# Kernel optimization log

Hardware: AMD Instinct MI355X
Metric: run time of the kernel (lower is better)

The kernel has to match this reference:

```python
import jax, jax.numpy as jnp
import numpy as np

D_MODEL = 1024
NUM_HEADS_Q = 16
NUM_HEADS_KV = 1
D_HEAD = D_MODEL // NUM_HEADS_Q  # 64
KV_DIM = D_HEAD * NUM_HEADS_KV   # 64


def setup_inputs() -> dict:
    key = jax.random.key(0)
    ks = jax.random.split(key, 9)
    b, n = 4, 2048
    s_in = 1.0 / np.sqrt(D_MODEL)
    s_o = 1.0 / np.sqrt(D_MODEL)
    return {
        "x": jax.random.normal(ks[0], (b, n, D_MODEL), jnp.float32),
        # weights stored as [in, out] (= torch Linear weight transposed)
        "W_q": jax.random.uniform(ks[1], (D_MODEL, D_MODEL), jnp.float32, -s_in, s_in),
        "b_q": jax.random.uniform(ks[2], (D_MODEL,), jnp.float32, -s_in, s_in),
        "W_k": jax.random.uniform(ks[3], (D_MODEL, KV_DIM), jnp.float32, -s_in, s_in),
        "b_k": jax.random.uniform(ks[4], (KV_DIM,), jnp.float32, -s_in, s_in),
        "W_v": jax.random.uniform(ks[5], (D_MODEL, KV_DIM), jnp.float32, -s_in, s_in),
        "b_v": jax.random.uniform(ks[6], (KV_DIM,), jnp.float32, -s_in, s_in),
        "W_o": jax.random.uniform(ks[7], (D_MODEL, D_MODEL), jnp.float32, -s_o, s_o),
        "b_o": jax.random.uniform(ks[8], (D_MODEL,), jnp.float32, -s_o, s_o),
    }


def reference(x, W_q, b_q, W_k, b_k, W_v, b_v, W_o, b_o):
    b, n, d_model = x.shape
    # projections
    q = (x @ W_q + b_q).reshape(b, n, NUM_HEADS_Q, D_HEAD).transpose(0, 2, 1, 3)  # [b,hq,n,dh]
    k = (x @ W_k + b_k).reshape(b, n, NUM_HEADS_KV, D_HEAD).transpose(0, 2, 1, 3)  # [b,hkv,n,dh]
    v = (x @ W_v + b_v).reshape(b, n, NUM_HEADS_KV, D_HEAD).transpose(0, 2, 1, 3)
    # MQA: single KV head broadcast over query heads via einsum broadcasting
    scale = 1.0 / np.sqrt(D_HEAD).astype(np.float32)
    # scores [b,hq,n,n]; k/v have hkv=1, broadcast over hq
    scores = jnp.einsum("bhqd,bknd->bhqn", q, k)[..., 0, :, :][:, :, None] if False else None
    # cleaner: squeeze kv head (num_heads_kv == 1)
    k1 = k[:, 0]  # [b,n,dh]
    v1 = v[:, 0]  # [b,n,dh]
    scores = jnp.einsum("bhqd,bkd->bhqk", q, k1) * scale  # [b,hq,n,n]
    attn = jax.nn.softmax(scores, axis=-1)
    out = jnp.einsum("bhqk,bkd->bhqd", attn, v1)  # [b,hq,n,dh]
    out = out.transpose(0, 2, 1, 3).reshape(b, n, d_model)
    return out @ W_o + b_o
```

## Files before the change

### kernel.cpp

```cpp
#include <hip/hip_runtime.h>

using bf16x8 = __attribute__((ext_vector_type(8))) short;
using f32x4  = __attribute__((ext_vector_type(4))) float;
using u32x2  = __attribute__((ext_vector_type(2))) unsigned int;

__device__ __forceinline__ unsigned short f2bf(float f) {
  unsigned int u = __float_as_uint(f);
  u = u + 0x7fffu + ((u >> 16) & 1u);
  return (unsigned short)(u >> 16);
}

#if __has_builtin(__builtin_amdgcn_exp2f)
#define EXP2(x) __builtin_amdgcn_exp2f(x)
#else
#define EXP2(x) __expf((x) * 0.69314718056f)
#endif

__device__ __forceinline__ unsigned int cvt_pk_bf16(float lo, float hi) {
  unsigned int r;
  asm("v_cvt_pk_bf16_f32 %0, %1, %2" : "=v"(r) : "v"(lo), "v"(hi));
  return r;
}

#define GLL16(SRC, DST) __builtin_amdgcn_global_load_lds( \
    (const __attribute__((address_space(1))) unsigned int*)(SRC), \
    (__attribute__((address_space(3))) unsigned int*)(DST), 16, 0, 0)

__global__ void cvt_x_kernel(const float* __restrict__ x, unsigned short* __restrict__ xb, int n4) {
  int i = blockIdx.x * blockDim.x + threadIdx.x;
  if (i >= n4) return;
  const float4 v = reinterpret_cast<const float4*>(x)[i];
  ushort2 o0 = { f2bf(v.x), f2bf(v.y) };
  ushort2 o1 = { f2bf(v.z), f2bf(v.w) };
  reinterpret_cast<ushort2*>(xb)[2 * i]     = o0;
  reinterpret_cast<ushort2*>(xb)[2 * i + 1] = o1;
}

__global__ __launch_bounds__(256) void cvt_wt_kernel(
    const float* __restrict__ W, unsigned short* __restrict__ Wt, int N, int K) {
  __shared__ float tile[32][33];
  const int n0 = blockIdx.x * 32, k0 = blockIdx.y * 32;
  const int tx = threadIdx.x & 31, ty = threadIdx.x >> 5;
  #pragma unroll
  for (int i = 0; i < 32; i += 8)
    tile[ty + i][tx] = W[(size_t)(k0 + ty + i) * N + n0 + tx];
  __syncthreads();
  #pragma unroll
  for (int i = 0; i < 32; i += 8)
    Wt[(size_t)(n0 + ty + i) * K + k0 + tx] = f2bf(tile[tx][ty + i]);
}

template<int MODE>
__global__ __launch_bounds__(256) void gemm_kernel(
    const unsigned short* __restrict__ A, const unsigned short* __restrict__ Bt,
    const float* __restrict__ bias0, const float* __restrict__ bias1,
    const float* __restrict__ bias2,
    void* __restrict__ out0, void* __restrict__ out1, void* __restrict__ out2,
    int K, int N) {
  __shared__ __align__(16) unsigned short alds[2][128 * 32];
  __shared__ __align__(16) unsigned short blds[2][128 * 32];

  const int t    = threadIdx.x;
  const int lane = t & 63;
  const int wid  = t >> 6;
  const int lr = lane & 15, lg = lane >> 4;
  const int row0 = blockIdx.x * 128;
  const int col0 = blockIdx.y * 128;

  const size_t ldb = (size_t)K * 2;
  const char* Ag = (const char*)A  + (size_t)(row0 + (t >> 2)) * ldb + ((t & 3) << 4);
  const char* Bg = (const char*)Bt + (size_t)(col0 + (t >> 2)) * ldb + ((t & 3) << 4);
  char* adst = (char*)alds[0] + wid * 1024;
  char* bdst = (char*)blds[0] + wid * 1024;

  auto stage = [&](int buf, int k0) {
    const size_t kb = (size_t)k0 * 2;
    #pragma unroll
    for (int c = 0; c < 2; ++c) {
      GLL16(Ag + (size_t)c * 64 * ldb + kb, adst + buf * 8192 + c * 4096);
      GLL16(Bg + (size_t)c * 64 * ldb + kb, bdst + buf * 8192 + c * 4096);
    }
  };

  f32x4 acc[4][4];
  #pragma unroll
  for (int i = 0; i < 4; ++i)
    #pragma unroll
    for (int j = 0; j < 4; ++j)
      #pragma unroll
      for (int r = 0; r < 4; ++r) acc[i][j][r] = 0.f;

  stage(0, 0);
  __syncthreads();

  for (int step = 0; step < 32; ++step) {
    const int cur = step & 1;
    if (step < 31) stage(cur ^ 1, (step + 1) * 32);

    const char* ab = (const char*)alds[cur] + (wid >> 1) * 4096;
    const char* bb = (const char*)blds[cur] + (wid & 1) * 4096;
    bf16x8 am[4], bn[4];
    #pragma unroll
    for (int i = 0; i < 4; ++i)
      am[i] = *reinterpret_cast<const bf16x8*>(ab + (i * 16 + lr) * 64 + lg * 16);
    #pragma unroll
    for (int j = 0; j < 4; ++j)
      bn[j] = *reinterpret_cast<const bf16x8*>(bb + (j * 16 + lr) * 64 + lg * 16);
    #pragma unroll
    for (int i = 0; i < 4; ++i)
      #pragma unroll
      for (int j = 0; j < 4; ++j)
        acc[i][j] = __builtin_amdgcn_mfma_f32_16x16x32_bf16(am[i], bn[j], acc[i][j], 0, 0, 0);

    __syncthreads();
  }

  const int wrow0 = row0 + (wid >> 1) * 64;
  const int wcol0 = col0 + (wid & 1) * 64;
  #pragma unroll
  for (int i = 0; i < 4; ++i) {
    #pragma unroll
    for (int j = 0; j < 4; ++j) {
      const int col = wcol0 + j * 16 + lr;
      float bias;
      if constexpr (MODE == 0)
        bias = (col < 1024) ? bias0[col] : ((col < 1088) ? bias1[col - 1024] : bias2[col - 1088]);
      else
        bias = bias0[col];
      #pragma unroll
      for (int r = 0; r < 4; ++r) {
        const int row = wrow0 + i * 16 + lg * 4 + r;
        float v = acc[i][j][r] + bias;
        if constexpr (MODE == 0) {
          const int b = row >> 11, n = row & 2047;
          if (col < 1024) {
            v *= 0.180336880111f;
            const int h = col >> 6, d = col & 63;
            ((unsigned short*)out0)[(((b * 16 + h) * 2048) + n) * 64 + d] = f2bf(v);
          } else if (col < 1088) {
            ((unsigned short*)out1)[row * 64 + (col - 1024)] = f2bf(v);
          } else {
            ((unsigned short*)out2)[(b * 64 + (col - 1088)) * 2048 + n] = f2bf(v);
          }
        } else {
          ((float*)out0)[(size_t)row * N + col] = v;
        }
      }
    }
  }
}

__global__ __launch_bounds__(512, 4) void attn_kernel(
    const unsigned short* __restrict__ Q,
    const unsigned short* __restrict__ Kb,
    const unsigned short* __restrict__ Vt,
    unsigned short* __restrict__ Ao) {
  __shared__ __align__(16) unsigned short klds[2][64 * 64];
  __shared__ __align__(16) unsigned short vlds[2][64 * 64];
  __shared__ __align__(16) unsigned short plds[8][32 * 64];

  const int lane = threadIdx.x & 63;
  const int wid  = threadIdx.x >> 6;
  const int lr = lane & 15, lg = lane >> 4;
  const int lr7x16 = (lr & 7) << 4;
  const int bh = blockIdx.y, b = bh >> 4, h = bh & 15;
  const int q0 = blockIdx.x * 256 + wid * 32;

  const unsigned short* Qb = Q + (size_t)bh * 2048 * 64;
  const char* Kbase = (const char*)(Kb + (size_t)b * 2048 * 64);
  const char* Vbase = (const char*)(Vt + (size_t)b * 64 * 2048);

  const int srow  = lane >> 3;
  const int schnk = (lane & 7) ^ (srow & 7);
  const int krow  = wid * 8 + srow;
  const int koff_lane = krow * 128  + schnk * 16;
  const int voff_lane = krow * 4096 + schnk * 16;
  char* kdst = (char*)klds[0] + wid * 1024;
  char* vdst = (char*)vlds[0] + wid * 1024;

  auto stage = [&](int buf, int kt) {
    GLL16(Kbase + (size_t)kt * 8192 + koff_lane, kdst + buf * 8192);
    GLL16(Vbase + (size_t)kt * 128  + voff_lane, vdst + buf * 8192);
  };

  bf16x8 qa[2][2];
  #pragma unroll
  for (int iq = 0; iq < 2; ++iq)
    #pragma unroll
    for (int kc = 0; kc < 2; ++kc)
      qa[iq][kc] = *reinterpret_cast<const bf16x8*>(
          &Qb[(q0 + iq * 16 + lr) * 64 + kc * 32 + lg * 8]);

  float lsum[2] = {0.f, 0.f};
  f32x4 o[2][4];
  #pragma unroll
  for (int iq = 0; iq < 2; ++iq)
    #pragma unroll
    for (int dt = 0; dt < 4; ++dt)
      #pragma unroll
      for (int r = 0; r < 4; ++r) o[iq][dt][r] = 0.f;

  stage(0, 0);
  __syncthreads();

  for (int kt = 0; kt < 32; ++kt) {
    const int cur = kt & 1;
    if (kt < 31) stage(cur ^ 1, kt + 1);

    const char* kb8 = (const char*)klds[cur];
    const char* vb8 = (const char*)vlds[cur];
    char* pw = (char*)plds[wid];

    f32x4 s[2][4];
    #pragma unroll
    for (int iq = 0; iq < 2; ++iq)
      #pragma unroll
      for (int ct = 0; ct < 4; ++ct)
        #pragma unroll
        for (int r = 0; r < 4; ++r) s[iq][ct][r] = 0.f;

    #pragma unroll
    for (int kc = 0; kc < 2; ++kc) {
      bf16x8 kf[4];
      #pragma unroll
      for (int ct = 0; ct < 4; ++ct)
        kf[ct] = *reinterpret_cast<const bf16x8*>(
            kb8 + ((ct * 16 + lr) << 7) + ((((kc << 2) + lg) << 4) ^ lr7x16));
      #pragma unroll
      for (int iq = 0; iq < 2; ++iq)
        #pragma unroll
        for (int ct = 0; ct < 4; ++ct)
          s[iq][ct] = __builtin_amdgcn_mfma_f32_16x16x32_bf16(kf[ct], qa[iq][kc], s[iq][ct], 0, 0, 0);
    }

    #pragma unroll
    for (int iq = 0; iq < 2; ++iq) {
      float ps = 0.f;
      const int rowb = (iq * 16 + lr) << 7;
      #pragma unroll
      for (int ct = 0; ct < 4; ++ct) {
        const float p0 = EXP2(s[iq][ct][0]);
        const float p1 = EXP2(s[iq][ct][1]);
        const float p2 = EXP2(s[iq][ct][2]);
        const float p3 = EXP2(s[iq][ct][3]);
        ps += (p0 + p1) + (p2 + p3);
        u32x2 pk2;
        pk2[0] = cvt_pk_bf16(p0, p1);
        pk2[1] = cvt_pk_bf16(p2, p3);
        const int chunkb = ((((ct << 1) + (lg >> 1)) << 4) ^ lr7x16) + ((lg & 1) << 3);
        *(u32x2*)(pw + rowb + chunkb) = pk2;
      }
      ps += __shfl_xor(ps, 16);
      ps += __shfl_xor(ps, 32);
      lsum[iq] += ps;
    }

    #pragma unroll
    for (int kc = 0; kc < 2; ++kc) {
      const int swz = (((kc << 2) + lg) << 4) ^ lr7x16;
      bf16x8 pb[2];
      #pragma unroll
      for (int iq = 0; iq < 2; ++iq)
        pb[iq] = *reinterpret_cast<const bf16x8*>(pw + ((iq * 16 + lr) << 7) + swz);
      bf16x8 vf[4];
      #pragma unroll
      for (int dt = 0; dt < 4; ++dt)
        vf[dt] = *reinterpret_cast<const bf16x8*>(vb8 + ((dt * 16 + lr) << 7) + swz);
      #pragma unroll
      for (int iq = 0; iq < 2; ++iq)
        #pragma unroll
        for (int dt = 0; dt < 4; ++dt)
          o[iq][dt] = __builtin_amdgcn_mfma_f32_16x16x32_bf16(vf[dt], pb[iq], o[iq][dt], 0, 0, 0);
    }

    __syncthreads();
  }

  #pragma unroll
  for (int iq = 0; iq < 2; ++iq) {
    const float inv = 1.f / lsum[iq];
    const size_t rowoff = (size_t)(b * 2048 + q0 + iq * 16 + lr) * 1024 + h * 64;
    #pragma unroll
    for (int dt = 0; dt < 4; ++dt) {
      u32x2 w;
      w[0] = cvt_pk_bf16(o[iq][dt][0] * inv, o[iq][dt][1] * inv);
      w[1] = cvt_pk_bf16(o[iq][dt][2] * inv, o[iq][dt][3] * inv);
      *(u32x2*)(Ao + rowoff + dt * 16 + lg * 4) = w;
    }
  }
}

extern "C" void kernel_launch(void* const* d_in, const int* in_sizes, int n_in,
                              void* d_out, int out_size, void* d_ws, size_t ws_size,
                              hipStream_t stream) {
  const float* x  = (const float*)d_in[0];
  const float* Wq = (const float*)d_in[1];
  const float* bq = (const float*)d_in[2];
  const float* Wk = (const float*)d_in[3];
  const float* bk = (const float*)d_in[4];
  const float* Wv = (const float*)d_in[5];
  const float* bv = (const float*)d_in[6];
  const float* Wo = (const float*)d_in[7];
  const float* bo = (const float*)d_in[8];
  float* out = (float*)d_out;

  char* ws = (char*)d_ws;
  size_t off = 0;
  auto alloc = [&](size_t bytes) -> void* {
    void* p = ws + off;
    off += (bytes + 255) & ~(size_t)255;
    return p;
  };
  unsigned short* xb    = (unsigned short*)alloc((size_t)8192 * 1024 * 2);
  unsigned short* wqkvt = (unsigned short*)alloc((size_t)1152 * 1024 * 2);
  unsigned short* wot   = (unsigned short*)alloc((size_t)1024 * 1024 * 2);
  unsigned short* qb    = (unsigned short*)alloc((size_t)8192 * 1024 * 2);
  unsigned short* kb    = (unsigned short*)alloc((size_t)8192 * 64 * 2);
  unsigned short* vt    = (unsigned short*)alloc((size_t)4 * 64 * 2048 * 2);
  unsigned short* ao    = (unsigned short*)alloc((size_t)8192 * 1024 * 2);

  cvt_x_kernel<<<8192, 256, 0, stream>>>(x, xb, 8192 * 1024 / 4);
  cvt_wt_kernel<<<dim3(32, 32), 256, 0, stream>>>(Wq, wqkvt, 1024, 1024);
  cvt_wt_kernel<<<dim3(2, 32), 256, 0, stream>>>(Wk, wqkvt + (size_t)1024 * 1024, 64, 1024);
  cvt_wt_kernel<<<dim3(2, 32), 256, 0, stream>>>(Wv, wqkvt + (size_t)1088 * 1024, 64, 1024);
  cvt_wt_kernel<<<dim3(32, 32), 256, 0, stream>>>(Wo, wot, 1024, 1024);

  gemm_kernel<0><<<dim3(64, 9), 256, 0, stream>>>(xb, wqkvt, bq, bk, bv, qb, kb, vt, 1024, 1152);
  attn_kernel<<<dim3(8, 64), 512, 0, stream>>>(qb, kb, vt, ao);
  gemm_kernel<2><<<dim3(64, 8), 256, 0, stream>>>(ao, wot, bo, nullptr, nullptr, out, nullptr, nullptr, 1024, 1024);
}
```

Before: 167.9 us.

## Use 32x32x16 MFMA for PV and load V fragments directly from global

The P·V product switches from 16x16x32 to 32x32x16 bf16 MFMA, so each wave issues fewer, larger matrix instructions with a 32-row accumulator layout. V is no longer staged through LDS; each wave reads its V fragments straight from global memory (L2-cached, shared across waves), which frees LDS and removes one async copy per tile. The row-sum shuffle reduction moves out of the inner loop to the epilogue. The trade-off is redundant global V reads across the 8 waves, with latency exposed inside the loop, in exchange for lower LDS traffic and MFMA issue overhead.

```diff
diff --git a/kernel.cpp b/kernel.cpp
--- a/kernel.cpp
+++ b/kernel.cpp
@@ -2,6 +2,7 @@
 
 using bf16x8 = __attribute__((ext_vector_type(8))) short;
 using f32x4  = __attribute__((ext_vector_type(4))) float;
+using f32x16 = __attribute__((ext_vector_type(16))) float;
 using u32x2  = __attribute__((ext_vector_type(2))) unsigned int;
 
 __device__ __forceinline__ unsigned short f2bf(float f) {
@@ -156,31 +157,28 @@
     const unsigned short* __restrict__ Vt,
     unsigned short* __restrict__ Ao) {
   __shared__ __align__(16) unsigned short klds[2][64 * 64];
-  __shared__ __align__(16) unsigned short vlds[2][64 * 64];
   __shared__ __align__(16) unsigned short plds[8][32 * 64];
 
   const int lane = threadIdx.x & 63;
   const int wid  = threadIdx.x >> 6;
   const int lr = lane & 15, lg = lane >> 4;
-  const int lr7x16 = (lr & 7) << 4;
+  const int la = lane & 31, hi = lane >> 5;
+  const int swzK = (lr & 7) << 4;
+  const int swzP = (la & 7) << 4;
   const int bh = blockIdx.y, b = bh >> 4, h = bh & 15;
   const int q0 = blockIdx.x * 256 + wid * 32;
 
   const unsigned short* Qb = Q + (size_t)bh * 2048 * 64;
   const char* Kbase = (const char*)(Kb + (size_t)b * 2048 * 64);
-  const char* Vbase = (const char*)(Vt + (size_t)b * 64 * 2048);
+  const unsigned short* Vg = Vt + (size_t)b * 64 * 2048;
 
   const int srow  = lane >> 3;
   const int schnk = (lane & 7) ^ (srow & 7);
-  const int krow  = wid * 8 + srow;
-  const int koff_lane = krow * 128  + schnk * 16;
-  const int voff_lane = krow * 4096 + schnk * 16;
+  const int koff_lane = (wid * 8 + srow) * 128 + schnk * 16;
   char* kdst = (char*)klds[0] + wid * 1024;
-  char* vdst = (char*)vlds[0] + wid * 1024;
 
   auto stage = [&](int buf, int kt) {
     GLL16(Kbase + (size_t)kt * 8192 + koff_lane, kdst + buf * 8192);
-    GLL16(Vbase + (size_t)kt * 128  + voff_lane, vdst + buf * 8192);
   };
 
   bf16x8 qa[2][2];
@@ -192,13 +190,11 @@
           &Qb[(q0 + iq * 16 + lr) * 64 + kc * 32 + lg * 8]);
 
   float lsum[2] = {0.f, 0.f};
-  f32x4 o[2][4];
-  #pragma unroll
-  for (int iq = 0; iq < 2; ++iq)
-    #pragma unroll
-    for (int dt = 0; dt < 4; ++dt)
-      #pragma unroll
-      for (int r = 0; r < 4; ++r) o[iq][dt][r] = 0.f;
+  f32x16 o[2];
+  #pragma unroll
+  for (int dt = 0; dt < 2; ++dt)
+    #pragma unroll
+    for (int r = 0; r < 16; ++r) o[dt][r] = 0.f;
 
   stage(0, 0);
   __syncthreads();
@@ -208,8 +204,15 @@
     if (kt < 31) stage(cur ^ 1, kt + 1);
 
     const char* kb8 = (const char*)klds[cur];
-    const char* vb8 = (const char*)vlds[cur];
     char* pw = (char*)plds[wid];
+
+    bf16x8 vf[4][2];
+    #pragma unroll
+    for (int s16 = 0; s16 < 4; ++s16)
+      #pragma unroll
+      for (int dt = 0; dt < 2; ++dt)
+        vf[s16][dt] = *reinterpret_cast<const bf16x8*>(
+            &Vg[(size_t)(dt * 32 + la) * 2048 + kt * 64 + s16 * 16 + hi * 8]);
 
     f32x4 s[2][4];
     #pragma unroll
@@ -225,7 +228,7 @@
       #pragma unroll
       for (int ct = 0; ct < 4; ++ct)
         kf[ct] = *reinterpret_cast<const bf16x8*>(
-            kb8 + ((ct * 16 + lr) << 7) + ((((kc << 2) + lg) << 4) ^ lr7x16));
+            kb8 + ((ct * 16 + lr) << 7) + ((((kc << 2) + lg) << 4) ^ swzK));
       #pragma unroll
       for (int iq = 0; iq < 2; ++iq)
         #pragma unroll
@@ -235,8 +238,8 @@
 
     #pragma unroll
     for (int iq = 0; iq < 2; ++iq) {
+      const int rowb = (iq * 16 + lr) << 7;
       float ps = 0.f;
-      const int rowb = (iq * 16 + lr) << 7;
       #pragma unroll
       for (int ct = 0; ct < 4; ++ct) {
         const float p0 = EXP2(s[iq][ct][0]);
@@ -247,45 +250,34 @@
         u32x2 pk2;
         pk2[0] = cvt_pk_bf16(p0, p1);
         pk2[1] = cvt_pk_bf16(p2, p3);
-        const int chunkb = ((((ct << 1) + (lg >> 1)) << 4) ^ lr7x16) + ((lg & 1) << 3);
-        *(u32x2*)(pw + rowb + chunkb) = pk2;
+        *(u32x2*)(pw + rowb + ((ct * 32 + lg * 8) ^ swzK)) = pk2;
       }
-      ps += __shfl_xor(ps, 16);
-      ps += __shfl_xor(ps, 32);
       lsum[iq] += ps;
     }
 
     #pragma unroll
-    for (int kc = 0; kc < 2; ++kc) {
-      const int swz = (((kc << 2) + lg) << 4) ^ lr7x16;
-      bf16x8 pb[2];
-      #pragma unroll
-      for (int iq = 0; iq < 2; ++iq)
-        pb[iq] = *reinterpret_cast<const bf16x8*>(pw + ((iq * 16 + lr) << 7) + swz);
-      bf16x8 vf[4];
-      #pragma unroll
-      for (int dt = 0; dt < 4; ++dt)
-        vf[dt] = *reinterpret_cast<const bf16x8*>(vb8 + ((dt * 16 + lr) << 7) + swz);
-      #pragma unroll
-      for (int iq = 0; iq < 2; ++iq)
-        #pragma unroll
-        for (int dt = 0; dt < 4; ++dt)
-          o[iq][dt] = __builtin_amdgcn_mfma_f32_16x16x32_bf16(vf[dt], pb[iq], o[iq][dt], 0, 0, 0);
+    for (int s16 = 0; s16 < 4; ++s16) {
+      const bf16x8 pb = *reinterpret_cast<const bf16x8*>(
+          pw + (la << 7) + (((s16 * 32) + (hi * 16)) ^ swzP));
+      o[0] = __builtin_amdgcn_mfma_f32_32x32x16_bf16(vf[s16][0], pb, o[0], 0, 0, 0);
+      o[1] = __builtin_amdgcn_mfma_f32_32x32x16_bf16(vf[s16][1], pb, o[1], 0, 0, 0);
     }
 
     __syncthreads();
   }
 
-  #pragma unroll
-  for (int iq = 0; iq < 2; ++iq) {
-    const float inv = 1.f / lsum[iq];
-    const size_t rowoff = (size_t)(b * 2048 + q0 + iq * 16 + lr) * 1024 + h * 64;
-    #pragma unroll
-    for (int dt = 0; dt < 4; ++dt) {
+  float t0 = lsum[0]; t0 += __shfl_xor(t0, 16); t0 += __shfl_xor(t0, 32);
+  float t1 = lsum[1]; t1 += __shfl_xor(t1, 16); t1 += __shfl_xor(t1, 32);
+  const float inv = 1.f / (la < 16 ? t0 : t1);
+  const size_t rowoff = (size_t)(b * 2048 + q0 + la) * 1024 + h * 64 + hi * 4;
+  #pragma unroll
+  for (int dt = 0; dt < 2; ++dt) {
+    #pragma unroll
+    for (int r2 = 0; r2 < 4; ++r2) {
       u32x2 w;
-      w[0] = cvt_pk_bf16(o[iq][dt][0] * inv, o[iq][dt][1] * inv);
-      w[1] = cvt_pk_bf16(o[iq][dt][2] * inv, o[iq][dt][3] * inv);
-      *(u32x2*)(Ao + rowoff + dt * 16 + lg * 4) = w;
+      w[0] = cvt_pk_bf16(o[dt][r2 * 4 + 0] * inv, o[dt][r2 * 4 + 1] * inv);
+      w[1] = cvt_pk_bf16(o[dt][r2 * 4 + 2] * inv, o[dt][r2 * 4 + 3] * inv);
+      *(u32x2*)(Ao + rowoff + dt * 32 + r2 * 8) = w;
     }
   }
 }
```

Result: slower. 249.6 us (+48.6%).
